# Kernel tuning notes

Hardware: AMD Instinct MI355X
Metric: run time of the kernel (lower is better)

Reference implementation:

```python
import jax, jax.numpy as jnp
import numpy as np

B, S, IN_DIM, HID, H, CS = 4, 4096, 1024, 1024, 16, 16
HD = HID // H
LN_EPS = 1e-5


def setup_inputs() -> dict:
    key = jax.random.key(0)
    ks = jax.random.split(key, 6)
    x = jax.random.normal(ks[0], (B, S, IN_DIM), jnp.float32)
    W_in = jax.random.normal(ks[1], (HID, IN_DIM), jnp.float32) * (IN_DIM ** -0.5)
    ln_g = jnp.ones((HID,), jnp.float32)
    ln_b = jnp.zeros((HID,), jnp.float32)
    W_gate = jax.random.normal(ks[2], (2 * H, HID), jnp.float32) * (HID ** -0.5)
    b_gate = jnp.zeros((2 * H,), jnp.float32)
    raw = 0.5 * float(np.log(1.9 / 0.1))  # atanh(0.9), as in _init_eigenvalues
    eig_raw = jnp.full((H,), raw, jnp.float32) + 0.01 * jax.random.normal(ks[3], (H,), jnp.float32)
    W_out = jax.random.normal(ks[4], (HID, HID), jnp.float32) * (HID ** -0.5)
    return {"x": x, "W_in": W_in, "ln_g": ln_g, "ln_b": ln_b,
            "W_gate": W_gate, "b_gate": b_gate, "eig_raw": eig_raw, "W_out": W_out}


def _chunk_scan(a, b):
    # a: (B,S,H) decay, b: (B,S,H,HD) input; h_t = a_t*h_{t-1} + b_t, h0 = 0
    Bsz, Sl = a.shape[0], a.shape[1]
    N = Sl // CS  # seq_len chosen divisible by chunk_size (pad_len == 0)
    ac = a.reshape(Bsz, N, CS, H)
    bc = b.reshape(Bsz, N, CS, H, HD)
    cum = jnp.cumprod(ac, axis=2)  # (B,N,C,H)
    ones = jnp.ones((Bsz, N, 1, H), a.dtype)
    cum_pad = jnp.concatenate([ones, cum[:, :, :-1]], axis=2)  # shifted cumprod
    # M[i,j] = cum_i / cum_pad_j for i>j, 1 on diag, 0 above
    Mi = cum[:, :, :, None, :]        # (B,N,C,1,H)
    Mj = cum_pad[:, :, None, :, :]    # (B,N,1,C,H)
    M = jnp.where(jnp.abs(Mj) > 1e-8, Mi / Mj, jnp.zeros_like(Mi))
    tril = jnp.tril(jnp.ones((CS, CS), a.dtype))[None, None, :, :, None]
    eye = jnp.eye(CS, dtype=a.dtype)[None, None, :, :, None]
    M = M * tril
    M = M * (1 - eye) + eye  # force exact 1 on diagonal
    # within-chunk contribution: (B,N,C,H,HD)
    h_contrib = jnp.einsum('bnijh,bnjhd->bnihd', M, bc)
    # inter-chunk sequential carry
    cum_T = jnp.moveaxis(cum, 1, 0)            # (N,B,C,H)
    hc_T = jnp.moveaxis(h_contrib, 1, 0)       # (N,B,C,H,HD)

    def step(h, inp):
        cum_n, hc_n = inp
        h_chunk = cum_n[..., None] * h[:, None] + hc_n  # (B,C,H,HD)
        return h_chunk[:, -1], h_chunk

    h0 = jnp.zeros((Bsz, H, HD), a.dtype)
    _, h_all = jax.lax.scan(step, h0, (cum_T, hc_T))   # (N,B,C,H,HD)
    h_all = jnp.moveaxis(h_all, 0, 1).reshape(Bsz, Sl, HID)
    return h_all


def reference(x, W_in, ln_g, ln_b, W_gate, b_gate, eig_raw, W_out):
    Bsz, Sl, _ = x.shape
    xp = x @ W_in.T                               # (B,S,HID)
    mu = jnp.mean(xp, axis=-1, keepdims=True)
    var = jnp.mean((xp - mu) ** 2, axis=-1, keepdims=True)
    xp = (xp - mu) * jax.lax.rsqrt(var + LN_EPS) * ln_g + ln_b
    gates = xp @ W_gate.T + b_gate                # (B,S,2H)
    alpha = jax.nn.sigmoid(gates[..., :H])
    beta = jax.nn.sigmoid(gates[..., H:])
    eig = jnp.tanh(eig_raw)                       # (H,)
    a = eig[None, None, :] * alpha                # (B,S,H)
    x_heads = xp.reshape(Bsz, Sl, H, HD)
    b = beta[..., None] * x_heads                 # (B,S,H,HD)
    h_all = _chunk_scan(a, b)                     # (B,S,HID)
    output = h_all @ W_out.T                      # dropout is identity in eval
    h_final = h_all[:, -1, :]
    return output, h_final
```

## Files before the change

### kernel.cpp

```cpp
#include <hip/hip_runtime.h>
#include <hip/hip_bf16.h>
#include <stdint.h>

#define BATCH 4
#define SEQ   4096
#define HID   1024
#define NH    16
#define HD    64
#define CS    16
#define NCH   256
#define MROWS 16384

typedef __attribute__((ext_vector_type(8))) __bf16 bf16x8;
typedef __attribute__((ext_vector_type(4))) float  f32x4;
typedef __attribute__((ext_vector_type(8))) unsigned short u16x8;

__device__ __forceinline__ unsigned short f2bf(float f) {
    union { float f; unsigned u; } x; x.f = f;
    unsigned r = x.u + 0x7FFFu + ((x.u >> 16) & 1u);
    return (unsigned short)(r >> 16);
}
__device__ __forceinline__ float bf2f(unsigned short v) {
    union { unsigned u; float f; } x; x.u = ((unsigned)v) << 16;
    return x.f;
}

__device__ __forceinline__ void async_copy16(void* lds, const void* g) {
    __builtin_amdgcn_global_load_lds(
        (const __attribute__((address_space(1))) unsigned int*)g,
        (__attribute__((address_space(3))) unsigned int*)lds,
        16, 0, 0);
}

__global__ __launch_bounds__(256) void convert_all_kernel(
    const float* __restrict__ x, const float* __restrict__ W_in,
    const float* __restrict__ W_out, const float* __restrict__ W_gate,
    unsigned short* __restrict__ xb, unsigned short* __restrict__ Wib,
    unsigned short* __restrict__ Wob, unsigned short* __restrict__ Wgb)
{
    int i = blockIdx.x * 256 + threadIdx.x;
    const float4* src; u16x8* dst; int j;
    if (i < 2097152)      { src = (const float4*)x;      dst = (u16x8*)xb;  j = i; }
    else if (i < 2228224) { src = (const float4*)W_in;   dst = (u16x8*)Wib; j = i - 2097152; }
    else if (i < 2359296) { src = (const float4*)W_out;  dst = (u16x8*)Wob; j = i - 2228224; }
    else if (i < 2363392) { src = (const float4*)W_gate; dst = (u16x8*)Wgb; j = i - 2359296; }
    else return;
    float4 a = src[2 * j], b = src[2 * j + 1];
    u16x8 o;
    o[0] = f2bf(a.x); o[1] = f2bf(a.y); o[2] = f2bf(a.z); o[3] = f2bf(a.w);
    o[4] = f2bf(b.x); o[5] = f2bf(b.y); o[6] = f2bf(b.z); o[7] = f2bf(b.w);
    dst[j] = o;
}

__global__ __launch_bounds__(256, 2) void gemm_bt_kernel(
    const unsigned short* __restrict__ A,
    const unsigned short* __restrict__ Bm,
    float* __restrict__ C, int M, int N, int K)
{
    __shared__ unsigned short As[128 * 64];
    __shared__ unsigned short Bs[128 * 64];
    const int t = threadIdx.x;
    const int lane = t & 63, w = t >> 6;
    const int wm = w >> 1, wn = w & 1;
    const size_t bm = (size_t)blockIdx.x * 128;
    const size_t bn = (size_t)blockIdx.y * 128;

    f32x4 acc[4][4];
#pragma unroll
    for (int x = 0; x < 4; x++)
#pragma unroll
        for (int y = 0; y < 4; y++)
            acc[x][y] = (f32x4){0.f, 0.f, 0.f, 0.f};

    const int srow = lane >> 3;
    const int gc   = (lane & 7) ^ (srow & 7);
    const int scol = gc * 8;
    const unsigned short* Ag = A + (bm + w * 32 + srow) * (size_t)K + scol;
    const unsigned short* Bg = Bm + (bn + w * 32 + srow) * (size_t)K + scol;
    unsigned short* Al = As + (w * 32 + srow) * 64 + (lane & 7) * 8;
    unsigned short* Bl = Bs + (w * 32 + srow) * 64 + (lane & 7) * 8;

    const int fr = lane & 15, fq = lane >> 4;
    const int rl = fr & 7;

    for (int k0 = 0; k0 < K; k0 += 64) {
#pragma unroll
        for (int r = 0; r < 4; r++) {
            async_copy16(Al + r * 8 * 64, Ag + (size_t)r * 8 * K + k0);
            async_copy16(Bl + r * 8 * 64, Bg + (size_t)r * 8 * K + k0);
        }
        __syncthreads();
#pragma unroll
        for (int kk = 0; kk < 64; kk += 32) {
            const int c = (kk >> 3) + fq;
            const int pc = c ^ rl;
            bf16x8 af[4], bfv[4];
#pragma unroll
            for (int x = 0; x < 4; x++) {
                af[x]  = *(const bf16x8*)(As + (wm * 64 + x * 16 + fr) * 64 + pc * 8);
                bfv[x] = *(const bf16x8*)(Bs + (wn * 64 + x * 16 + fr) * 64 + pc * 8);
            }
#pragma unroll
            for (int x = 0; x < 4; x++)
#pragma unroll
                for (int y = 0; y < 4; y++)
                    acc[x][y] = __builtin_amdgcn_mfma_f32_16x16x32_bf16(af[x], bfv[y], acc[x][y], 0, 0, 0);
        }
        __syncthreads();
    }

#pragma unroll
    for (int x = 0; x < 4; x++) {
#pragma unroll
        for (int y = 0; y < 4; y++) {
            size_t r0 = bm + wm * 64 + x * 16 + fq * 4;
            size_t c  = bn + wn * 64 + y * 16 + fr;
#pragma unroll
            for (int rg = 0; rg < 4; rg++)
                C[(r0 + rg) * (size_t)N + c] = acc[x][y][rg];
        }
    }
}

__global__ __launch_bounds__(256) void ln_kernel(
    const float* __restrict__ xp, const float* __restrict__ ln_g,
    const float* __restrict__ ln_b, unsigned short* __restrict__ xln)
{
    const int row  = blockIdx.x * 4 + (threadIdx.x >> 6);
    const int lane = threadIdx.x & 63;
    const float* rp = xp + (size_t)row * 1024;
    float4 va[2], vb[2];
    float s = 0.f, s2 = 0.f;
#pragma unroll
    for (int i = 0; i < 2; i++) {
        const int k = lane * 8 + i * 512;
        va[i] = *(const float4*)(rp + k);
        vb[i] = *(const float4*)(rp + k + 4);
        s  += va[i].x + va[i].y + va[i].z + va[i].w
            + vb[i].x + vb[i].y + vb[i].z + vb[i].w;
        s2 += va[i].x * va[i].x + va[i].y * va[i].y + va[i].z * va[i].z + va[i].w * va[i].w
            + vb[i].x * vb[i].x + vb[i].y * vb[i].y + vb[i].z * vb[i].z + vb[i].w * vb[i].w;
    }
#pragma unroll
    for (int off = 1; off < 64; off <<= 1) {
        s  += __shfl_xor(s, off, 64);
        s2 += __shfl_xor(s2, off, 64);
    }
    const float mu  = s * (1.f / 1024.f);
    const float var = s2 * (1.f / 1024.f) - mu * mu;
    const float sc  = rsqrtf(var + 1e-5f);
    unsigned short* orow = xln + (size_t)row * 1024;
#pragma unroll
    for (int i = 0; i < 2; i++) {
        const int k = lane * 8 + i * 512;
        float4 g4a = *(const float4*)(ln_g + k);
        float4 g4b = *(const float4*)(ln_g + k + 4);
        float4 b4a = *(const float4*)(ln_b + k);
        float4 b4b = *(const float4*)(ln_b + k + 4);
        u16x8 o;
        o[0] = f2bf((va[i].x - mu) * sc * g4a.x + b4a.x);
        o[1] = f2bf((va[i].y - mu) * sc * g4a.y + b4a.y);
        o[2] = f2bf((va[i].z - mu) * sc * g4a.z + b4a.z);
        o[3] = f2bf((va[i].w - mu) * sc * g4a.w + b4a.w);
        o[4] = f2bf((vb[i].x - mu) * sc * g4b.x + b4b.x);
        o[5] = f2bf((vb[i].y - mu) * sc * g4b.y + b4b.y);
        o[6] = f2bf((vb[i].z - mu) * sc * g4b.z + b4b.z);
        o[7] = f2bf((vb[i].w - mu) * sc * g4b.w + b4b.w);
        *(u16x8*)(orow + k) = o;
    }
}

__global__ __launch_bounds__(256) void gates_kernel(
    const unsigned short* __restrict__ xln,
    const unsigned short* __restrict__ Wgb,
    const float* __restrict__ bg, const float* __restrict__ eig_raw,
    float* __restrict__ beta_buf,
    float* __restrict__ cum_out,
    float* __restrict__ c15c,
    float* __restrict__ hc15)
{
    __shared__ unsigned short sx[16][1032];
    __shared__ float red[4][2][64][4];
    __shared__ float sg[16][32];
    __shared__ float scum[16][16];
    const int t = threadIdx.x, lane = t & 63, w = t >> 6;
    const int bn = blockIdx.x;
    const size_t m0 = (size_t)(bn >> 8) * SEQ + (size_t)(bn & 255) * 16;
    const int r = t >> 4, u = t & 15;

    {
        const unsigned short* xrow = xln + (m0 + r) * 1024;
#pragma unroll
        for (int i = 0; i < 8; i++) {
            const int k = u * 8 + i * 128;
            *(u16x8*)&sx[r][k] = *(const u16x8*)(xrow + k);
        }
    }
    __syncthreads();

    const int fr = lane & 15, fq = lane >> 4;
    {
        f32x4 acc0 = (f32x4){0.f,0.f,0.f,0.f}, acc1 = (f32x4){0.f,0.f,0.f,0.f};
        const unsigned short* Wr0 = Wgb + (size_t)fr * 1024;
        const unsigned short* Wr1 = Wgb + (size_t)(16 + fr) * 1024;
#pragma unroll
        for (int ks = 0; ks < 8; ks++) {
            const int k0 = w * 256 + ks * 32 + fq * 8;
            bf16x8 af = *(const bf16x8*)&sx[fr][k0];
            bf16x8 b0 = *(const bf16x8*)(Wr0 + k0);
            bf16x8 b1 = *(const bf16x8*)(Wr1 + k0);
            acc0 = __builtin_amdgcn_mfma_f32_16x16x32_bf16(af, b0, acc0, 0, 0, 0);
            acc1 = __builtin_amdgcn_mfma_f32_16x16x32_bf16(af, b1, acc1, 0, 0, 0);
        }
        *(f32x4*)&red[w][0][lane][0] = acc0;
        *(f32x4*)&red[w][1][lane][0] = acc1;
    }
    __syncthreads();
    if (t < 128) {
        const int y = t >> 6, l = t & 63;
        f32x4 s = *(const f32x4*)&red[0][y][l][0];
#pragma unroll
        for (int ww = 1; ww < 4; ww++) {
            f32x4 p = *(const f32x4*)&red[ww][y][l][0];
            s[0] += p[0]; s[1] += p[1]; s[2] += p[2]; s[3] += p[3];
        }
        const int col = y * 16 + (l & 15);
        const int row0 = (l >> 4) * 4;
        const float bias = bg[col];
#pragma unroll
        for (int rg = 0; rg < 4; rg++)
            sg[row0 + rg][col] = 1.f / (1.f + expf(-(s[rg] + bias)));
    }
    __syncthreads();

    if (t < 16) {
        const float ev = tanhf(eig_raw[t]);
        float c = 1.f;
#pragma unroll
        for (int i = 0; i < 16; i++) { c *= ev * sg[i][t]; scum[i][t] = c; }
    }
    beta_buf[(m0 + r) * 16 + u] = sg[r][16 + u];
    __syncthreads();

    cum_out[(size_t)bn * 256 + t] = scum[t >> 4][t & 15];
    if (t < 16) c15c[bn * 16 + t] = scum[15][t];

    {
        const int h = t >> 4, d0 = (t & 15) * 4;
        float s0 = 0.f, s1 = 0.f, s2 = 0.f, s3 = 0.f;
        float b0 = 0.f, b1 = 0.f, b2 = 0.f, b3 = 0.f;
        float cprev = 1.f;
#pragma unroll
        for (int j = 0; j < 16; j++) {
            const float bt = sg[j][16 + h];
            ushort4 xv = *(const ushort4*)&sx[j][h * 64 + d0];
            b0 = bt * bf2f(xv.x); b1 = bt * bf2f(xv.y);
            b2 = bt * bf2f(xv.z); b3 = bt * bf2f(xv.w);
            if (j < 15) {
                const float inv = (fabsf(cprev) > 1e-8f) ? (1.f / cprev) : 0.f;
                s0 += b0 * inv; s1 += b1 * inv; s2 += b2 * inv; s3 += b3 * inv;
                cprev = scum[j][h];
            }
        }
        const float c15 = scum[15][h];
        float4 o = { c15 * s0 + b0, c15 * s1 + b1, c15 * s2 + b2, c15 * s3 + b3 };
        *(float4*)(hc15 + (size_t)bn * 1024 + h * 64 + d0) = o;
    }
}

__global__ __launch_bounds__(256) void scan2a_kernel(
    const float* __restrict__ c15c,
    const float* __restrict__ hc15,
    float* __restrict__ Pg,
    float* __restrict__ Sg)
{
    const int tid = blockIdx.x * 256 + threadIdx.x;
    const int b = tid >> 14, g = (tid >> 10) & 15, hd = tid & 1023, h = hd >> 6;
    const int n0 = b * NCH + g * 16;
    float P = 1.f, S = 0.f;
#pragma unroll
    for (int j = 0; j < 16; j++) {
        const float c = c15c[(n0 + j) * 16 + h];
        S = c * S + hc15[(size_t)(n0 + j) * 1024 + hd];
        P = c * P;
    }
    Pg[tid] = P;
    Sg[tid] = S;
}

__global__ __launch_bounds__(128) void scan3_kernel(
    const float* __restrict__ cum_buf,
    const float* __restrict__ beta_buf,
    const unsigned short* __restrict__ xln,
    const float* __restrict__ c15c,
    const float* __restrict__ hc15,
    const float* __restrict__ Pg,
    const float* __restrict__ Sg,
    unsigned short* __restrict__ hall,
    float* __restrict__ h_final)
{
    __shared__ float scum[16][16];
    __shared__ float sbeta[16][16];
    const int t = threadIdx.x;
    const int bn = blockIdx.x;
    const int b = bn >> 8, n = bn & 255, g = n >> 4;
    const size_t m0 = (size_t)b * SEQ + (size_t)n * 16;

    {
        const int i0 = t, i1 = t + 128;
        scum[i0 >> 4][i0 & 15]  = cum_buf[(size_t)bn * 256 + i0];
        scum[i1 >> 4][i1 & 15]  = cum_buf[(size_t)bn * 256 + i1];
        sbeta[i0 >> 4][i0 & 15] = beta_buf[(m0 + (i0 >> 4)) * 16 + (i0 & 15)];
        sbeta[i1 >> 4][i1 & 15] = beta_buf[(m0 + (i1 >> 4)) * 16 + (i1 & 15)];
    }
    __syncthreads();

    const int h = t >> 3, dq = t & 7;
    const size_t off = h * 64 + dq * 8;

    float s[8];
#pragma unroll
    for (int e = 0; e < 8; e++) s[e] = 0.f;
    for (int gp = 0; gp < g; gp++) {
        const size_t idx = ((size_t)(b * 16 + gp) << 10) + off;
        float4 p0 = *(const float4*)(Pg + idx), p1 = *(const float4*)(Pg + idx + 4);
        float4 q0 = *(const float4*)(Sg + idx), q1 = *(const float4*)(Sg + idx + 4);
        s[0] = p0.x * s[0] + q0.x; s[1] = p0.y * s[1] + q0.y;
        s[2] = p0.z * s[2] + q0.z; s[3] = p0.w * s[3] + q0.w;
        s[4] = p1.x * s[4] + q1.x; s[5] = p1.y * s[5] + q1.y;
        s[6] = p1.z * s[6] + q1.z; s[7] = p1.w * s[7] + q1.w;
    }
    for (int jj = (g << 4); jj < n; jj++) {
        const size_t cn = (size_t)b * 256 + jj;
        const float c = c15c[cn * 16 + h];
        float4 h0 = *(const float4*)(hc15 + cn * 1024 + off);
        float4 h1 = *(const float4*)(hc15 + cn * 1024 + off + 4);
        s[0] = c * s[0] + h0.x; s[1] = c * s[1] + h0.y;
        s[2] = c * s[2] + h0.z; s[3] = c * s[3] + h0.w;
        s[4] = c * s[4] + h1.x; s[5] = c * s[5] + h1.y;
        s[6] = c * s[6] + h1.z; s[7] = c * s[7] + h1.w;
    }
    if (n == 255) {
        const size_t cn = (size_t)b * 256 + 255;
        const float c = c15c[cn * 16 + h];
        float4 h0 = *(const float4*)(hc15 + cn * 1024 + off);
        float4 h1 = *(const float4*)(hc15 + cn * 1024 + off + 4);
        float4 f0 = { c * s[0] + h0.x, c * s[1] + h0.y, c * s[2] + h0.z, c * s[3] + h0.w };
        float4 f1 = { c * s[4] + h1.x, c * s[5] + h1.y, c * s[6] + h1.z, c * s[7] + h1.w };
        *(float4*)(h_final + ((size_t)b << 10) + off)     = f0;
        *(float4*)(h_final + ((size_t)b << 10) + off + 4) = f1;
    }

    float cprev = 1.f;
#pragma unroll
    for (int i = 0; i < 16; i++) {
        u16x8 xv = *(const u16x8*)(xln + (m0 + i) * 1024 + off);
        const float bt = sbeta[i][h];
        const float ci = scum[i][h];
        float bb[8];
        u16x8 o;
#pragma unroll
        for (int e = 0; e < 8; e++) {
            bb[e] = bt * bf2f(xv[e]);
            o[e] = f2bf(ci * s[e] + bb[e]);
        }
        *(u16x8*)(hall + (m0 + i) * 1024 + off) = o;
        const float inv = (fabsf(cprev) > 1e-8f) ? (1.f / cprev) : 0.f;
#pragma unroll
        for (int e = 0; e < 8; e++)
            s[e] += bb[e] * inv;
        cprev = ci;
    }
}

extern "C" void kernel_launch(void* const* d_in, const int* in_sizes, int n_in,
                              void* d_out, int out_size, void* d_ws, size_t ws_size,
                              hipStream_t stream)
{
    const float* x       = (const float*)d_in[0];
    const float* W_in    = (const float*)d_in[1];
    const float* ln_g    = (const float*)d_in[2];
    const float* ln_b    = (const float*)d_in[3];
    const float* W_gate  = (const float*)d_in[4];
    const float* b_gate  = (const float*)d_in[5];
    const float* eig_raw = (const float*)d_in[6];
    const float* W_out   = (const float*)d_in[7];
    float* out = (float*)d_out;

    char* ws = (char*)d_ws;
    unsigned short* xb   = (unsigned short*)(ws);
    unsigned short* xln  = (unsigned short*)(ws);
    unsigned short* hall = (unsigned short*)(ws + 33554432);
    unsigned short* Wib  = (unsigned short*)(ws + 67108864);
    unsigned short* Wob  = (unsigned short*)(ws + 69206016);
    unsigned short* Wgb  = (unsigned short*)(ws + 71303168);
    float* beta_buf = (float*)(ws + 71368704);
    float* cum_buf  = (float*)(ws + 72417280);
    float* c15c     = (float*)(ws + 73465856);
    float* hc15     = (float*)(ws + 73531392);
    float* Pg = (float*)(ws + 77725696);
    float* Sg = (float*)(ws + 77725696 + 262144);

    float* xp = out;
    float* h_final = out + 16777216;

    convert_all_kernel<<<9232, 256, 0, stream>>>(x, W_in, W_out, W_gate, xb, Wib, Wob, Wgb);

    dim3 gg(128, 8);
    gemm_bt_kernel<<<gg, 256, 0, stream>>>(xb, Wib, xp, MROWS, HID, HID);

    ln_kernel<<<4096, 256, 0, stream>>>(xp, ln_g, ln_b, xln);

    gates_kernel<<<1024, 256, 0, stream>>>(xln, Wgb, b_gate, eig_raw,
                                           beta_buf, cum_buf, c15c, hc15);

    scan2a_kernel<<<256, 256, 0, stream>>>(c15c, hc15, Pg, Sg);

    scan3_kernel<<<1024, 128, 0, stream>>>(cum_buf, beta_buf, xln, c15c, hc15,
                                           Pg, Sg, hall, h_final);

    gemm_bt_kernel<<<gg, 256, 0, stream>>>(hall, Wob, out, MROWS, HID, HID);
}
```

Baseline: 254.3 us.

## Rewrite gates kernel as single-wavefront block using shuffles; raise GEMM occupancy hint

The gates kernel now runs one 64-lane wavefront per 16-row chunk. It accumulates the full K dimension in registers, so the LDS staging, cross-wave reduction and all __syncthreads barriers are gone. The cumulative decay product is built with lane shuffles, and each lane reads its x values straight from global memory for the within-chunk carry. The GEMM launch bound is also raised to 4 blocks per CU, which may cap registers and cause spills in exchange for occupancy.

```diff
diff --git a/kernel.cpp b/kernel.cpp
--- a/kernel.cpp
+++ b/kernel.cpp
@@ -52,7 +52,7 @@
     dst[j] = o;
 }
 
-__global__ __launch_bounds__(256, 2) void gemm_bt_kernel(
+__global__ __launch_bounds__(256, 4) void gemm_bt_kernel(
     const unsigned short* __restrict__ A,
     const unsigned short* __restrict__ Bm,
     float* __restrict__ C, int M, int N, int K)
@@ -170,7 +170,7 @@
     }
 }
 
-__global__ __launch_bounds__(256) void gates_kernel(
+__global__ __launch_bounds__(64) void gates_kernel(
     const unsigned short* __restrict__ xln,
     const unsigned short* __restrict__ Wgb,
     const float* __restrict__ bg, const float* __restrict__ eig_raw,
@@ -179,93 +179,95 @@
     float* __restrict__ c15c,
     float* __restrict__ hc15)
 {
-    __shared__ unsigned short sx[16][1032];
-    __shared__ float red[4][2][64][4];
-    __shared__ float sg[16][32];
-    __shared__ float scum[16][16];
-    const int t = threadIdx.x, lane = t & 63, w = t >> 6;
+    const int lane = threadIdx.x;
     const int bn = blockIdx.x;
     const size_t m0 = (size_t)(bn >> 8) * SEQ + (size_t)(bn & 255) * 16;
-    const int r = t >> 4, u = t & 15;
-
+    const int fr = lane & 15, fq = lane >> 4;
+
+    f32x4 acc0 = (f32x4){0.f,0.f,0.f,0.f}, acc1 = (f32x4){0.f,0.f,0.f,0.f};
     {
-        const unsigned short* xrow = xln + (m0 + r) * 1024;
-#pragma unroll
-        for (int i = 0; i < 8; i++) {
-            const int k = u * 8 + i * 128;
-            *(u16x8*)&sx[r][k] = *(const u16x8*)(xrow + k);
-        }
-    }
-    __syncthreads();
-
-    const int fr = lane & 15, fq = lane >> 4;
-    {
-        f32x4 acc0 = (f32x4){0.f,0.f,0.f,0.f}, acc1 = (f32x4){0.f,0.f,0.f,0.f};
+        const unsigned short* Xr  = xln + (m0 + fr) * 1024;
         const unsigned short* Wr0 = Wgb + (size_t)fr * 1024;
         const unsigned short* Wr1 = Wgb + (size_t)(16 + fr) * 1024;
-#pragma unroll
-        for (int ks = 0; ks < 8; ks++) {
-            const int k0 = w * 256 + ks * 32 + fq * 8;
-            bf16x8 af = *(const bf16x8*)&sx[fr][k0];
+#pragma unroll 8
+        for (int ks = 0; ks < 32; ks++) {
+            const int k0 = ks * 32 + fq * 8;
+            bf16x8 af = *(const bf16x8*)(Xr + k0);
             bf16x8 b0 = *(const bf16x8*)(Wr0 + k0);
             bf16x8 b1 = *(const bf16x8*)(Wr1 + k0);
             acc0 = __builtin_amdgcn_mfma_f32_16x16x32_bf16(af, b0, acc0, 0, 0, 0);
             acc1 = __builtin_amdgcn_mfma_f32_16x16x32_bf16(af, b1, acc1, 0, 0, 0);
         }
-        *(f32x4*)&red[w][0][lane][0] = acc0;
-        *(f32x4*)&red[w][1][lane][0] = acc1;
-    }
-    __syncthreads();
-    if (t < 128) {
-        const int y = t >> 6, l = t & 63;
-        f32x4 s = *(const f32x4*)&red[0][y][l][0];
-#pragma unroll
-        for (int ww = 1; ww < 4; ww++) {
-            f32x4 p = *(const f32x4*)&red[ww][y][l][0];
-            s[0] += p[0]; s[1] += p[1]; s[2] += p[2]; s[3] += p[3];
-        }
-        const int col = y * 16 + (l & 15);
-        const int row0 = (l >> 4) * 4;
-        const float bias = bg[col];
-#pragma unroll
-        for (int rg = 0; rg < 4; rg++)
-            sg[row0 + rg][col] = 1.f / (1.f + expf(-(s[rg] + bias)));
-    }
-    __syncthreads();
-
-    if (t < 16) {
-        const float ev = tanhf(eig_raw[t]);
-        float c = 1.f;
-#pragma unroll
-        for (int i = 0; i < 16; i++) { c *= ev * sg[i][t]; scum[i][t] = c; }
-    }
-    beta_buf[(m0 + r) * 16 + u] = sg[r][16 + u];
-    __syncthreads();
-
-    cum_out[(size_t)bn * 256 + t] = scum[t >> 4][t & 15];
-    if (t < 16) c15c[bn * 16 + t] = scum[15][t];
-
-    {
-        const int h = t >> 4, d0 = (t & 15) * 4;
-        float s0 = 0.f, s1 = 0.f, s2 = 0.f, s3 = 0.f;
-        float b0 = 0.f, b1 = 0.f, b2 = 0.f, b3 = 0.f;
-        float cprev = 1.f;
-#pragma unroll
-        for (int j = 0; j < 16; j++) {
-            const float bt = sg[j][16 + h];
-            ushort4 xv = *(const ushort4*)&sx[j][h * 64 + d0];
-            b0 = bt * bf2f(xv.x); b1 = bt * bf2f(xv.y);
-            b2 = bt * bf2f(xv.z); b3 = bt * bf2f(xv.w);
-            if (j < 15) {
-                const float inv = (fabsf(cprev) > 1e-8f) ? (1.f / cprev) : 0.f;
-                s0 += b0 * inv; s1 += b1 * inv; s2 += b2 * inv; s3 += b3 * inv;
-                cprev = scum[j][h];
-            }
-        }
-        const float c15 = scum[15][h];
-        float4 o = { c15 * s0 + b0, c15 * s1 + b1, c15 * s2 + b2, c15 * s3 + b3 };
-        *(float4*)(hc15 + (size_t)bn * 1024 + h * 64 + d0) = o;
-    }
+    }
+    const float bA = bg[fr], bB = bg[16 + fr];
+    const float ev = tanhf(eig_raw[fr]);
+    float av[4], bt[4];
+#pragma unroll
+    for (int rg = 0; rg < 4; rg++) {
+        av[rg] = ev / (1.f + expf(-(acc0[rg] + bA)));
+        bt[rg] = 1.f / (1.f + expf(-(acc1[rg] + bB)));
+    }
+
+    const float l0 = av[0], l1 = l0 * av[1], l2 = l1 * av[2], l3 = l2 * av[3];
+    const float p0 = __shfl(l3, fr);
+    const float p1 = __shfl(l3, fr + 16);
+    const float p2 = __shfl(l3, fr + 32);
+    float pre = 1.f;
+    if (fq >= 1) pre *= p0;
+    if (fq >= 2) pre *= p1;
+    if (fq >= 3) pre *= p2;
+    float sc[4] = { pre * l0, pre * l1, pre * l2, pre * l3 };
+    const float c15all = __shfl(sc[3], fr + 48);
+
+#pragma unroll
+    for (int rg = 0; rg < 4; rg++) {
+        cum_out[(size_t)bn * 256 + (fq * 4 + rg) * 16 + fr] = sc[rg];
+        beta_buf[(m0 + fq * 4 + rg) * 16 + fr] = bt[rg];
+    }
+    if (fq == 0) c15c[bn * 16 + fr] = c15all;
+
+    const int h = lane >> 2, dq = lane & 3;
+    float btj[16], scj[16];
+#pragma unroll
+    for (int q = 0; q < 4; q++)
+#pragma unroll
+        for (int rg = 0; rg < 4; rg++) {
+            btj[q * 4 + rg] = __shfl(bt[rg], q * 16 + h);
+            scj[q * 4 + rg] = __shfl(sc[rg], q * 16 + h);
+        }
+
+    const size_t off = (size_t)h * 64 + dq * 16;
+    float s[16], bb[16];
+#pragma unroll
+    for (int e = 0; e < 16; e++) s[e] = 0.f;
+    float cprev = 1.f;
+#pragma unroll
+    for (int j = 0; j < 16; j++) {
+        const unsigned short* xr = xln + (m0 + j) * 1024 + off;
+        u16x8 xv0 = *(const u16x8*)(xr);
+        u16x8 xv1 = *(const u16x8*)(xr + 8);
+        const float btv = btj[j];
+#pragma unroll
+        for (int e = 0; e < 8; e++) {
+            bb[e]     = btv * bf2f(xv0[e]);
+            bb[8 + e] = btv * bf2f(xv1[e]);
+        }
+        if (j < 15) {
+            const float inv = (fabsf(cprev) > 1e-8f) ? (1.f / cprev) : 0.f;
+#pragma unroll
+            for (int e = 0; e < 16; e++) s[e] += bb[e] * inv;
+            cprev = scj[j];
+        }
+    }
+    const float c15h = scj[15];
+    float ov[16];
+#pragma unroll
+    for (int e = 0; e < 16; e++) ov[e] = c15h * s[e] + bb[e];
+    float* hp = hc15 + (size_t)bn * 1024 + off;
+    *(float4*)(hp)      = *(float4*)&ov[0];
+    *(float4*)(hp + 4)  = *(float4*)&ov[4];
+    *(float4*)(hp + 8)  = *(float4*)&ov[8];
+    *(float4*)(hp + 12) = *(float4*)&ov[12];
 }
 
 __global__ __launch_bounds__(256) void scan2a_kernel(
@@ -411,8 +413,8 @@
 
     ln_kernel<<<4096, 256, 0, stream>>>(xp, ln_g, ln_b, xln);
 
-    gates_kernel<<<1024, 256, 0, stream>>>(xln, Wgb, b_gate, eig_raw,
-                                           beta_buf, cum_buf, c15c, hc15);
+    gates_kernel<<<1024, 64, 0, stream>>>(xln, Wgb, b_gate, eig_raw,
+                                          beta_buf, cum_buf, c15c, hc15);
 
     scan2a_kernel<<<256, 256, 0, stream>>>(c15c, hc15, Pg, Sg);
 
```

Measured after the change: 262.5 us. 3.2% more time.

## Fuse LayerNorm statistics into input GEMM epilogue and apply norm inside gates kernel

Applied to the files above, without the earlier changes.

The input projection GEMM now reduces per-row sum and sum of squares in its epilogue and accumulates them with atomics into a stats buffer. That buffer is zeroed inside the conversion kernel. The standalone LayerNorm kernel is removed: the gates kernel reads the fp32 projection, normalizes it, fills its shared tile and writes the bf16 normalized activations for later use. This drops one kernel launch and one full read pass over the fp32 projection, at the cost of atomics and slightly more epilogue work in the GEMM.

```diff
diff --git a/kernel.cpp b/kernel.cpp
--- a/kernel.cpp
+++ b/kernel.cpp
@@ -36,7 +36,8 @@
     const float* __restrict__ x, const float* __restrict__ W_in,
     const float* __restrict__ W_out, const float* __restrict__ W_gate,
     unsigned short* __restrict__ xb, unsigned short* __restrict__ Wib,
-    unsigned short* __restrict__ Wob, unsigned short* __restrict__ Wgb)
+    unsigned short* __restrict__ Wob, unsigned short* __restrict__ Wgb,
+    float* __restrict__ stats)
 {
     int i = blockIdx.x * 256 + threadIdx.x;
     const float4* src; u16x8* dst; int j;
@@ -44,6 +45,10 @@
     else if (i < 2228224) { src = (const float4*)W_in;   dst = (u16x8*)Wib; j = i - 2097152; }
     else if (i < 2359296) { src = (const float4*)W_out;  dst = (u16x8*)Wob; j = i - 2228224; }
     else if (i < 2363392) { src = (const float4*)W_gate; dst = (u16x8*)Wgb; j = i - 2359296; }
+    else if (i < 2371584) {
+        ((float4*)stats)[i - 2363392] = (float4){0.f, 0.f, 0.f, 0.f};
+        return;
+    }
     else return;
     float4 a = src[2 * j], b = src[2 * j + 1];
     u16x8 o;
@@ -122,58 +127,108 @@
     }
 }
 
-__global__ __launch_bounds__(256) void ln_kernel(
-    const float* __restrict__ xp, const float* __restrict__ ln_g,
-    const float* __restrict__ ln_b, unsigned short* __restrict__ xln)
-{
-    const int row  = blockIdx.x * 4 + (threadIdx.x >> 6);
-    const int lane = threadIdx.x & 63;
-    const float* rp = xp + (size_t)row * 1024;
-    float4 va[2], vb[2];
-    float s = 0.f, s2 = 0.f;
-#pragma unroll
-    for (int i = 0; i < 2; i++) {
-        const int k = lane * 8 + i * 512;
-        va[i] = *(const float4*)(rp + k);
-        vb[i] = *(const float4*)(rp + k + 4);
-        s  += va[i].x + va[i].y + va[i].z + va[i].w
-            + vb[i].x + vb[i].y + vb[i].z + vb[i].w;
-        s2 += va[i].x * va[i].x + va[i].y * va[i].y + va[i].z * va[i].z + va[i].w * va[i].w
-            + vb[i].x * vb[i].x + vb[i].y * vb[i].y + vb[i].z * vb[i].z + vb[i].w * vb[i].w;
-    }
-#pragma unroll
-    for (int off = 1; off < 64; off <<= 1) {
-        s  += __shfl_xor(s, off, 64);
-        s2 += __shfl_xor(s2, off, 64);
-    }
-    const float mu  = s * (1.f / 1024.f);
-    const float var = s2 * (1.f / 1024.f) - mu * mu;
-    const float sc  = rsqrtf(var + 1e-5f);
-    unsigned short* orow = xln + (size_t)row * 1024;
-#pragma unroll
-    for (int i = 0; i < 2; i++) {
-        const int k = lane * 8 + i * 512;
-        float4 g4a = *(const float4*)(ln_g + k);
-        float4 g4b = *(const float4*)(ln_g + k + 4);
-        float4 b4a = *(const float4*)(ln_b + k);
-        float4 b4b = *(const float4*)(ln_b + k + 4);
-        u16x8 o;
-        o[0] = f2bf((va[i].x - mu) * sc * g4a.x + b4a.x);
-        o[1] = f2bf((va[i].y - mu) * sc * g4a.y + b4a.y);
-        o[2] = f2bf((va[i].z - mu) * sc * g4a.z + b4a.z);
-        o[3] = f2bf((va[i].w - mu) * sc * g4a.w + b4a.w);
-        o[4] = f2bf((vb[i].x - mu) * sc * g4b.x + b4b.x);
-        o[5] = f2bf((vb[i].y - mu) * sc * g4b.y + b4b.y);
-        o[6] = f2bf((vb[i].z - mu) * sc * g4b.z + b4b.z);
-        o[7] = f2bf((vb[i].w - mu) * sc * g4b.w + b4b.w);
-        *(u16x8*)(orow + k) = o;
+__global__ __launch_bounds__(256, 2) void gemm_bt_stats_kernel(
+    const unsigned short* __restrict__ A,
+    const unsigned short* __restrict__ Bm,
+    float* __restrict__ C,
+    float* __restrict__ stat_sum, float* __restrict__ stat_sqs,
+    int M, int N, int K)
+{
+    __shared__ unsigned short As[128 * 64];
+    __shared__ unsigned short Bs[128 * 64];
+    const int t = threadIdx.x;
+    const int lane = t & 63, w = t >> 6;
+    const int wm = w >> 1, wn = w & 1;
+    const size_t bm = (size_t)blockIdx.x * 128;
+    const size_t bn = (size_t)blockIdx.y * 128;
+
+    f32x4 acc[4][4];
+#pragma unroll
+    for (int x = 0; x < 4; x++)
+#pragma unroll
+        for (int y = 0; y < 4; y++)
+            acc[x][y] = (f32x4){0.f, 0.f, 0.f, 0.f};
+
+    const int srow = lane >> 3;
+    const int gc   = (lane & 7) ^ (srow & 7);
+    const int scol = gc * 8;
+    const unsigned short* Ag = A + (bm + w * 32 + srow) * (size_t)K + scol;
+    const unsigned short* Bg = Bm + (bn + w * 32 + srow) * (size_t)K + scol;
+    unsigned short* Al = As + (w * 32 + srow) * 64 + (lane & 7) * 8;
+    unsigned short* Bl = Bs + (w * 32 + srow) * 64 + (lane & 7) * 8;
+
+    const int fr = lane & 15, fq = lane >> 4;
+    const int rl = fr & 7;
+
+    for (int k0 = 0; k0 < K; k0 += 64) {
+#pragma unroll
+        for (int r = 0; r < 4; r++) {
+            async_copy16(Al + r * 8 * 64, Ag + (size_t)r * 8 * K + k0);
+            async_copy16(Bl + r * 8 * 64, Bg + (size_t)r * 8 * K + k0);
+        }
+        __syncthreads();
+#pragma unroll
+        for (int kk = 0; kk < 64; kk += 32) {
+            const int c = (kk >> 3) + fq;
+            const int pc = c ^ rl;
+            bf16x8 af[4], bfv[4];
+#pragma unroll
+            for (int x = 0; x < 4; x++) {
+                af[x]  = *(const bf16x8*)(As + (wm * 64 + x * 16 + fr) * 64 + pc * 8);
+                bfv[x] = *(const bf16x8*)(Bs + (wn * 64 + x * 16 + fr) * 64 + pc * 8);
+            }
+#pragma unroll
+            for (int x = 0; x < 4; x++)
+#pragma unroll
+                for (int y = 0; y < 4; y++)
+                    acc[x][y] = __builtin_amdgcn_mfma_f32_16x16x32_bf16(af[x], bfv[y], acc[x][y], 0, 0, 0);
+        }
+        __syncthreads();
+    }
+
+#pragma unroll
+    for (int x = 0; x < 4; x++) {
+#pragma unroll
+        for (int y = 0; y < 4; y++) {
+            size_t r0 = bm + wm * 64 + x * 16 + fq * 4;
+            size_t c  = bn + wn * 64 + y * 16 + fr;
+#pragma unroll
+            for (int rg = 0; rg < 4; rg++)
+                C[(r0 + rg) * (size_t)N + c] = acc[x][y][rg];
+        }
+    }
+
+#pragma unroll
+    for (int x = 0; x < 4; x++) {
+#pragma unroll
+        for (int rg = 0; rg < 4; rg++) {
+            float ps = 0.f, pq = 0.f;
+#pragma unroll
+            for (int y = 0; y < 4; y++) {
+                const float v = acc[x][y][rg];
+                ps += v; pq += v * v;
+            }
+#pragma unroll
+            for (int off = 1; off < 16; off <<= 1) {
+                ps += __shfl_xor(ps, off, 64);
+                pq += __shfl_xor(pq, off, 64);
+            }
+            if (fr == 0) {
+                const size_t row = bm + wm * 64 + x * 16 + fq * 4 + rg;
+                atomicAdd(&stat_sum[row], ps);
+                atomicAdd(&stat_sqs[row], pq);
+            }
+        }
     }
 }
 
 __global__ __launch_bounds__(256) void gates_kernel(
-    const unsigned short* __restrict__ xln,
+    const float* __restrict__ xp,
+    const float* __restrict__ stat_sum, const float* __restrict__ stat_sqs,
+    const float* __restrict__ ln_g, const float* __restrict__ ln_b,
     const unsigned short* __restrict__ Wgb,
     const float* __restrict__ bg, const float* __restrict__ eig_raw,
+    unsigned short* __restrict__ xln,
     float* __restrict__ beta_buf,
     float* __restrict__ cum_out,
     float* __restrict__ c15c,
@@ -189,11 +244,24 @@
     const int r = t >> 4, u = t & 15;
 
     {
-        const unsigned short* xrow = xln + (m0 + r) * 1024;
-#pragma unroll
-        for (int i = 0; i < 8; i++) {
-            const int k = u * 8 + i * 128;
-            *(u16x8*)&sx[r][k] = *(const u16x8*)(xrow + k);
+        const float* row = xp + (m0 + r) * 1024;
+        const float mu  = stat_sum[m0 + r] * (1.f / 1024.f);
+        const float var = stat_sqs[m0 + r] * (1.f / 1024.f) - mu * mu;
+        const float sc  = rsqrtf(var + 1e-5f);
+        unsigned short* orow = xln + (m0 + r) * 1024;
+#pragma unroll
+        for (int i = 0; i < 16; i++) {
+            const int k = u * 4 + i * 64;
+            float4 v  = *(const float4*)(row + k);
+            float4 g4 = *(const float4*)(ln_g + k);
+            float4 b4 = *(const float4*)(ln_b + k);
+            ushort4 o;
+            o.x = f2bf((v.x - mu) * sc * g4.x + b4.x);
+            o.y = f2bf((v.y - mu) * sc * g4.y + b4.y);
+            o.z = f2bf((v.z - mu) * sc * g4.z + b4.z);
+            o.w = f2bf((v.w - mu) * sc * g4.w + b4.w);
+            *(ushort4*)&sx[r][k] = o;
+            *(ushort4*)(orow + k) = o;
         }
     }
     __syncthreads();
@@ -398,21 +466,24 @@
     float* cum_buf  = (float*)(ws + 72417280);
     float* c15c     = (float*)(ws + 73465856);
     float* hc15     = (float*)(ws + 73531392);
-    float* Pg = (float*)(ws + 77725696);
-    float* Sg = (float*)(ws + 77725696 + 262144);
+    float* Pg       = (float*)(ws + 77725696);
+    float* Sg       = (float*)(ws + 77725696 + 262144);
+    float* stat_sum = (float*)(ws + 77725696 + 524288);
+    float* stat_sqs = (float*)(ws + 77725696 + 589824);
 
     float* xp = out;
     float* h_final = out + 16777216;
 
-    convert_all_kernel<<<9232, 256, 0, stream>>>(x, W_in, W_out, W_gate, xb, Wib, Wob, Wgb);
+    convert_all_kernel<<<9264, 256, 0, stream>>>(x, W_in, W_out, W_gate,
+                                                 xb, Wib, Wob, Wgb, stat_sum);
 
     dim3 gg(128, 8);
-    gemm_bt_kernel<<<gg, 256, 0, stream>>>(xb, Wib, xp, MROWS, HID, HID);
-
-    ln_kernel<<<4096, 256, 0, stream>>>(xp, ln_g, ln_b, xln);
-
-    gates_kernel<<<1024, 256, 0, stream>>>(xln, Wgb, b_gate, eig_raw,
-                                           beta_buf, cum_buf, c15c, hc15);
+    gemm_bt_stats_kernel<<<gg, 256, 0, stream>>>(xb, Wib, xp, stat_sum, stat_sqs,
+                                                 MROWS, HID, HID);
+
+    gates_kernel<<<1024, 256, 0, stream>>>(xp, stat_sum, stat_sqs, ln_g, ln_b,
+                                           Wgb, b_gate, eig_raw,
+                                           xln, beta_buf, cum_buf, c15c, hc15);
 
     scan2a_kernel<<<256, 256, 0, stream>>>(c15c, hc15, Pg, Sg);
 
```

Measured after the change: 262.6 us. +3.3%, slower.
